# Optimization experiments

Measured on AMD Instinct MI355X. Metric: run time of the kernel, lower is better.

Reference implementation:

```python
import jax, jax.numpy as jnp
import numpy as np

N_NODES = 50000
N_EDGES = 800000
F_IN = 128
HID = 128
N_GRAPHS = 256


def setup_inputs() -> dict:
    key = jax.random.key(0)
    ks = jax.random.split(key, 12)
    gx = jax.random.normal(ks[0], (N_NODES, F_IN), dtype=jnp.float32)
    edge_index = jax.random.randint(ks[1], (2, N_EDGES), 0, N_NODES, dtype=jnp.int64)
    batch = jnp.sort(jax.random.randint(ks[2], (N_NODES,), 0, N_GRAPHS, dtype=jnp.int64))
    edge_attr = jax.random.uniform(ks[3], (N_EDGES,), dtype=jnp.float32)
    s1 = 1.0 / np.sqrt(F_IN)
    s2 = 1.0 / np.sqrt(HID)
    W1 = jax.random.uniform(ks[4], (F_IN, HID), jnp.float32, -s1, s1)
    b1 = jnp.zeros((HID,), jnp.float32)
    W2 = jax.random.uniform(ks[5], (HID, HID), jnp.float32, -s2, s2)
    b2 = jnp.zeros((HID,), jnp.float32)
    W3 = jax.random.uniform(ks[6], (HID, HID), jnp.float32, -s2, s2)
    b3 = jnp.zeros((HID,), jnp.float32)
    return {"gx": gx, "edge_index": edge_index, "batch": batch, "edge_attr": edge_attr,
            "W1": W1, "b1": b1, "W2": W2, "b2": b2, "W3": W3, "b3": b3}


def _gcn_conv(x, W, b, row, col, edge_weight, n_nodes):
    # PyG GCNConv with add_self_loops=False:
    #   deg[i] = sum of edge_weight over edges with dst == i
    #   norm_e = deg^{-1/2}[row] * w_e * deg^{-1/2}[col]
    #   out[i] = sum_{e: col_e == i} norm_e * (x @ W)[row_e] + b
    deg = jax.ops.segment_sum(edge_weight, col, num_segments=n_nodes)
    dinv = jnp.where(deg > 0, jax.lax.rsqrt(deg), 0.0)
    norm = dinv[row] * edge_weight * dinv[col]  # [E]
    h = x @ W  # [N, H]
    msg = h[row] * norm[:, None]  # [E, H] gather + scale
    out = jax.ops.segment_sum(msg, col, num_segments=n_nodes)  # scatter-add
    return out + b


def reference(gx, edge_index, batch, edge_attr, W1, b1, W2, b2, W3, b3):
    row, col = edge_index[0], edge_index[1]
    n = gx.shape[0]
    # dropout layers are in eval mode (identity) for a deterministic reference
    h = jax.nn.relu(_gcn_conv(gx, W1, b1, row, col, edge_attr, n))
    h = jax.nn.relu(_gcn_conv(h, W2, b2, row, col, edge_attr, n))
    h = _gcn_conv(h, W3, b3, row, col, edge_attr, n)
    readout = jax.ops.segment_sum(h, batch, num_segments=N_GRAPHS)  # global_add_pool
    return h, readout
```

## Files before the change

### kernel.cpp

```cpp
#include <hip/hip_runtime.h>

#define FEAT 128

typedef __attribute__((ext_vector_type(8))) short short8;
typedef __attribute__((ext_vector_type(4))) float f32x4;

__device__ __forceinline__ unsigned int bf16rtn(float f) {
    unsigned int u = __float_as_uint(f);
    return (u + 0x7fffu + ((u >> 16) & 1u)) >> 16;
}
__device__ __forceinline__ float bf16tof(unsigned int h) { return __uint_as_float(h << 16); }
__device__ __forceinline__ float bf16lo(unsigned int v) { return __uint_as_float(v << 16); }
__device__ __forceinline__ float bf16hi(unsigned int v) { return __uint_as_float(v & 0xffff0000u); }

__global__ void zero_kernel(float* __restrict__ p, int n) {
    int i = blockIdx.x * blockDim.x + threadIdx.x;
    if (i < n) p[i] = 0.0f;
}

__global__ __launch_bounds__(256) void hist_kernel(const int* __restrict__ col,
                                                   int* __restrict__ ghist,
                                                   int E, int nblk, int nbuck) {
    __shared__ int h[256];
    const int t = threadIdx.x, b = blockIdx.x;
    h[t] = 0;
    __syncthreads();
    const int base = b * 4096;
#pragma unroll
    for (int i = 0; i < 16; ++i) {
        int e = base + i * 256 + t;
        if (e < E) atomicAdd(&h[col[e] >> 8], 1);
    }
    __syncthreads();
    if (t < nbuck) ghist[t * nblk + b] = h[t];
}

__global__ __launch_bounds__(256) void scan_block_kernel(const int* __restrict__ cnt,
                                                         int* __restrict__ out,
                                                         int* __restrict__ bsum, int M) {
    __shared__ int s[256];
    int t = threadIdx.x;
    int i = blockIdx.x * 256 + t;
    int own = (i < M) ? cnt[i] : 0;
    s[t] = own;
    for (int off = 1; off < 256; off <<= 1) {
        __syncthreads();
        int v = (t >= off) ? s[t - off] : 0;
        __syncthreads();
        s[t] += v;
    }
    __syncthreads();
    if (i < M) out[i] = s[t] - own;
    if (t == 255) bsum[blockIdx.x] = s[255];
}

__global__ __launch_bounds__(256) void scan_bsum_kernel(int* __restrict__ bsum, int nb) {
    __shared__ int s[256];
    int t = threadIdx.x;
    int own = (t < nb) ? bsum[t] : 0;
    s[t] = own;
    for (int off = 1; off < 256; off <<= 1) {
        __syncthreads();
        int v = (t >= off) ? s[t - off] : 0;
        __syncthreads();
        s[t] += v;
    }
    __syncthreads();
    if (t < nb) bsum[t] = s[t] - own;
}

__global__ __launch_bounds__(256) void scan_add_kernel(int* __restrict__ out,
                                                       const int* __restrict__ bsum,
                                                       int M, int total) {
    int i = blockIdx.x * 256 + threadIdx.x;
    if (i < M) out[i] += bsum[blockIdx.x];
    if (i == M) out[M] = total;
}

__global__ __launch_bounds__(256) void scatter1_kernel(const int* __restrict__ row,
                                                       const int* __restrict__ col,
                                                       const float* __restrict__ ew,
                                                       const int* __restrict__ gbase,
                                                       uint2* __restrict__ bedge,
                                                       int E, int nblk, int nbuck) {
    __shared__ int cur[256];
    const int t = threadIdx.x, b = blockIdx.x;
    if (t < nbuck) cur[t] = gbase[t * nblk + b];
    __syncthreads();
    const int base = b * 4096;
#pragma unroll
    for (int i = 0; i < 16; ++i) {
        int e = base + i * 256 + t;
        if (e < E) {
            int c = col[e];
            int slot = atomicAdd(&cur[c >> 8], 1);
            bedge[slot] = make_uint2(((unsigned)c << 16) | (unsigned)row[e],
                                     __float_as_uint(ew[e]));
        }
    }
}

__global__ __launch_bounds__(256) void bucket_kernel(const uint2* __restrict__ bedge,
                                                     const int* __restrict__ gbase,
                                                     int* __restrict__ rowptr,
                                                     float* __restrict__ dinv,
                                                     uint2* __restrict__ sedge,
                                                     int N, int E, int nblk, int nbuck) {
    __shared__ int lcnt[256];
    __shared__ float lw[256];
    __shared__ int lscan[256];
    __shared__ int lcur[256];
    __shared__ float ldv[256];

    const int d = blockIdx.x, t = threadIdx.x;
    const int base = gbase[d * nblk];
    const int end  = (d == nbuck - 1) ? E : gbase[(d + 1) * nblk];

    lcnt[t] = 0;
    lw[t] = 0.f;
    __syncthreads();
    for (int i = base + t; i < end; i += 256) {
        uint2 p = bedge[i];
        int c = (p.x >> 16) & 255;
        atomicAdd(&lcnt[c], 1);
        atomicAdd(&lw[c], __uint_as_float(p.y));
    }
    __syncthreads();
    int own = lcnt[t];
    lscan[t] = own;
    for (int off = 1; off < 256; off <<= 1) {
        __syncthreads();
        int v = (t >= off) ? lscan[t - off] : 0;
        __syncthreads();
        lscan[t] += v;
    }
    __syncthreads();
    int excl = lscan[t] - own;
    lcur[t] = base + excl;
    float wsum = lw[t];
    float dv = (wsum > 0.f) ? rsqrtf(wsum) : 0.f;
    ldv[t] = dv;
    int node = d * 256 + t;
    if (node < N) {
        rowptr[node] = base + excl;
        dinv[node] = dv;
    }
    if (d == nbuck - 1 && t == 0) rowptr[N] = E;
    __syncthreads();
    for (int i = base + t; i < end; i += 256) {
        uint2 p = bedge[i];
        int c = (p.x >> 16) & 255;
        int slot = atomicAdd(&lcur[c], 1);
        sedge[slot] = make_uint2(p.x & 0xFFFFu,
                                 __float_as_uint(__uint_as_float(p.y) * ldv[c]));
    }
}

__global__ void norm_kernel(uint2* __restrict__ sedge, const float* __restrict__ dinv, int E) {
    int i = blockIdx.x * blockDim.x + threadIdx.x;
    if (i < E) {
        uint2 p = sedge[i];
        p.y = __float_as_uint(__uint_as_float(p.y) * dinv[p.x]);
        sedge[i] = p;
    }
}

__global__ void convw_kernel(const float* __restrict__ W0, const float* __restrict__ W1,
                             const float* __restrict__ W2,
                             unsigned short* __restrict__ Whi, unsigned short* __restrict__ Wlo) {
    int i = blockIdx.x * blockDim.x + threadIdx.x;
    int which = blockIdx.y;
    const float* W = (which == 0) ? W0 : (which == 1) ? W1 : W2;
    int c = i >> 7, k = i & 127;
    float w = W[(size_t)k * FEAT + c];
    unsigned int h = bf16rtn(w);
    size_t off = (size_t)which * 16384 + (size_t)c * FEAT + k;
    Whi[off] = (unsigned short)h;
    Wlo[off] = (unsigned short)bf16rtn(w - bf16tof(h));
}

__global__ __launch_bounds__(256) void gemm_mfma_kernel(
    const float* __restrict__ X,
    const unsigned short* __restrict__ Wthi, const unsigned short* __restrict__ Wtlo,
    unsigned int* __restrict__ hb,
    int N)
{
    __shared__ unsigned short xh[64 * 128];
    __shared__ unsigned short xl[64 * 128];
    __shared__ unsigned short wh[64 * 128];
    __shared__ unsigned short wl[64 * 128];

    const int tid = threadIdx.x;
    const int r0 = blockIdx.x * 64;
    const int cb = blockIdx.y;

#pragma unroll
    for (int it = 0; it < 4; ++it) {
        int idx = it * 256 + tid;
        int c = idx >> 4;
        int k8 = (idx & 15) * 8;
        int sw = k8 ^ ((c & 7) << 3);
        size_t src = (size_t)(cb * 64 + c) * FEAT + k8;
        *(short8*)&wh[c * 128 + sw] = *(const short8*)(Wthi + src);
        *(short8*)&wl[c * 128 + sw] = *(const short8*)(Wtlo + src);
    }
#pragma unroll
    for (int it = 0; it < 8; ++it) {
        int idx = it * 256 + tid;
        int r = idx >> 5;
        int kc = (idx & 31) * 4;
        int gr = r0 + r;
        float4 v = make_float4(0.f, 0.f, 0.f, 0.f);
        if (gr < N) v = *(const float4*)(X + (size_t)gr * FEAT + kc);
        unsigned int h0 = bf16rtn(v.x), h1 = bf16rtn(v.y);
        unsigned int h2 = bf16rtn(v.z), h3 = bf16rtn(v.w);
        ushort4 hv = make_ushort4((unsigned short)h0, (unsigned short)h1,
                                  (unsigned short)h2, (unsigned short)h3);
        ushort4 lv = make_ushort4((unsigned short)bf16rtn(v.x - bf16tof(h0)),
                                  (unsigned short)bf16rtn(v.y - bf16tof(h1)),
                                  (unsigned short)bf16rtn(v.z - bf16tof(h2)),
                                  (unsigned short)bf16rtn(v.w - bf16tof(h3)));
        int sw = kc ^ ((r & 7) << 3);
        *(ushort4*)&xh[r * 128 + sw] = hv;
        *(ushort4*)&xl[r * 128 + sw] = lv;
    }
    __syncthreads();

    const int lane = tid & 63;
    const int wv = tid >> 6;
    const int m = lane & 15;
    const int quad = lane >> 4;
    const int arow = wv * 16 + m;

    f32x4 acc[4];
#pragma unroll
    for (int ct = 0; ct < 4; ++ct) acc[ct] = (f32x4){0.f, 0.f, 0.f, 0.f};

#pragma unroll
    for (int kt = 0; kt < 4; ++kt) {
        const int k0 = kt * 32 + quad * 8;
        const int aw = k0 ^ ((arow & 7) << 3);
        short8 ah = *(const short8*)&xh[arow * 128 + aw];
        short8 al = *(const short8*)&xl[arow * 128 + aw];
#pragma unroll
        for (int ct = 0; ct < 4; ++ct) {
            int bc = ct * 16 + m;
            int bw = k0 ^ ((bc & 7) << 3);
            short8 bh = *(const short8*)&wh[bc * 128 + bw];
            short8 bl = *(const short8*)&wl[bc * 128 + bw];
            acc[ct] = __builtin_amdgcn_mfma_f32_16x16x32_bf16(ah, bh, acc[ct], 0, 0, 0);
            acc[ct] = __builtin_amdgcn_mfma_f32_16x16x32_bf16(ah, bl, acc[ct], 0, 0, 0);
            acc[ct] = __builtin_amdgcn_mfma_f32_16x16x32_bf16(al, bh, acc[ct], 0, 0, 0);
        }
    }

    __syncthreads();
    unsigned short* cl = xh;
#pragma unroll
    for (int ct = 0; ct < 4; ++ct)
#pragma unroll
        for (int reg = 0; reg < 4; ++reg) {
            int rrow = wv * 16 + quad * 4 + reg;
            cl[rrow * 72 + ct * 16 + m] = (unsigned short)bf16rtn(acc[ct][reg]);
        }
    __syncthreads();
#pragma unroll
    for (int it = 0; it < 2; ++it) {
        int idx = it * 256 + tid;
        int r = idx >> 3;
        int c4 = (idx & 7) * 4;
        int gr = r0 + r;
        if (gr < N) {
            uint4 pv = *(const uint4*)&cl[r * 72 + c4 * 2];
            *(uint4*)(hb + (size_t)gr * 64 + cb * 32 + c4) = pv;
        }
    }
}

template <int RELU>
__global__ __launch_bounds__(256) void agg_kernel(
    const int* __restrict__ rowptr, const uint2* __restrict__ sedge,
    const unsigned int* __restrict__ hb, const float* __restrict__ bias,
    float* __restrict__ outX, int N)
{
    const int node = blockIdx.x * 4 + (threadIdx.x >> 6);
    if (node >= N) return;
    const int lane = threadIdx.x & 63;
    const int s = rowptr[node];
    const int e = rowptr[node + 1];

    float2 bv = *(const float2*)(bias + lane * 2);
    float a0 = bv.x, a1 = bv.y;

    int i = s;
    const int nfull = (e - s) >> 3;
    if (nfull > 0) {
        uint2 c0 = sedge[i], c1 = sedge[i + 1], c2 = sedge[i + 2], c3 = sedge[i + 3];
        uint2 c4 = sedge[i + 4], c5 = sedge[i + 5], c6 = sedge[i + 6], c7 = sedge[i + 7];
        for (int g = 0; g < nfull; ++g) {
            unsigned v0 = hb[(size_t)c0.x * 64 + lane];
            unsigned v1 = hb[(size_t)c1.x * 64 + lane];
            unsigned v2 = hb[(size_t)c2.x * 64 + lane];
            unsigned v3 = hb[(size_t)c3.x * 64 + lane];
            unsigned v4 = hb[(size_t)c4.x * 64 + lane];
            unsigned v5 = hb[(size_t)c5.x * 64 + lane];
            unsigned v6 = hb[(size_t)c6.x * 64 + lane];
            unsigned v7 = hb[(size_t)c7.x * 64 + lane];
            float w0 = __uint_as_float(c0.y), w1 = __uint_as_float(c1.y);
            float w2 = __uint_as_float(c2.y), w3 = __uint_as_float(c3.y);
            float w4 = __uint_as_float(c4.y), w5 = __uint_as_float(c5.y);
            float w6 = __uint_as_float(c6.y), w7 = __uint_as_float(c7.y);
            int ni = i + 8;
            if (g + 1 < nfull) {
                c0 = sedge[ni];     c1 = sedge[ni + 1];
                c2 = sedge[ni + 2]; c3 = sedge[ni + 3];
                c4 = sedge[ni + 4]; c5 = sedge[ni + 5];
                c6 = sedge[ni + 6]; c7 = sedge[ni + 7];
            }
            a0 = fmaf(w0, bf16lo(v0), a0);  a1 = fmaf(w0, bf16hi(v0), a1);
            a0 = fmaf(w1, bf16lo(v1), a0);  a1 = fmaf(w1, bf16hi(v1), a1);
            a0 = fmaf(w2, bf16lo(v2), a0);  a1 = fmaf(w2, bf16hi(v2), a1);
            a0 = fmaf(w3, bf16lo(v3), a0);  a1 = fmaf(w3, bf16hi(v3), a1);
            a0 = fmaf(w4, bf16lo(v4), a0);  a1 = fmaf(w4, bf16hi(v4), a1);
            a0 = fmaf(w5, bf16lo(v5), a0);  a1 = fmaf(w5, bf16hi(v5), a1);
            a0 = fmaf(w6, bf16lo(v6), a0);  a1 = fmaf(w6, bf16hi(v6), a1);
            a0 = fmaf(w7, bf16lo(v7), a0);  a1 = fmaf(w7, bf16hi(v7), a1);
            i = ni;
        }
    }
    for (; i < e; ++i) {
        uint2 p = sedge[i];
        unsigned v = hb[(size_t)p.x * 64 + lane];
        float w = __uint_as_float(p.y);
        a0 = fmaf(w, bf16lo(v), a0);
        a1 = fmaf(w, bf16hi(v), a1);
    }

    if (RELU) { a0 = fmaxf(a0, 0.f); a1 = fmaxf(a1, 0.f); }
    *(float2*)(outX + (size_t)node * FEAT + lane * 2) = make_float2(a0, a1);
}

__global__ __launch_bounds__(128) void readout_kernel(const float* __restrict__ h,
                                                      const int* __restrict__ batch,
                                                      float* __restrict__ ro, int N) {
    const int g = blockIdx.x;
    const int chunk = blockIdx.y;
    const int j = threadIdx.x;
    int lo = 0, hi = N;
    while (lo < hi) { int mid = (lo + hi) >> 1; if (batch[mid] < g) lo = mid + 1; else hi = mid; }
    int lo2 = lo, hi2 = N;
    while (lo2 < hi2) { int mid = (lo2 + hi2) >> 1; if (batch[mid] < g + 1) lo2 = mid + 1; else hi2 = mid; }
    const int len = lo2 - lo;
    const int per = (len + 7) >> 3;
    const int cs = lo + chunk * per;
    const int ce = min(lo2, cs + per);

    float s0 = 0.f, s1 = 0.f, s2 = 0.f, s3 = 0.f;
    int n = cs;
    for (; n + 4 <= ce; n += 4) {
        s0 += h[(size_t)n * FEAT + j];
        s1 += h[(size_t)(n + 1) * FEAT + j];
        s2 += h[(size_t)(n + 2) * FEAT + j];
        s3 += h[(size_t)(n + 3) * FEAT + j];
    }
    for (; n < ce; ++n) s0 += h[(size_t)n * FEAT + j];
    float acc = (s0 + s1) + (s2 + s3);
    if (cs < ce) atomicAdd(&ro[(size_t)g * FEAT + j], acc);
}

static inline size_t align256(size_t x) { return (x + 255) & ~(size_t)255; }

extern "C" void kernel_launch(void* const* d_in, const int* in_sizes, int n_in,
                              void* d_out, int out_size, void* d_ws, size_t ws_size,
                              hipStream_t stream) {
    const float* gx    = (const float*)d_in[0];
    const int*   ei    = (const int*)d_in[1];
    const int*   batch = (const int*)d_in[2];
    const float* ew    = (const float*)d_in[3];
    const float* W1 = (const float*)d_in[4];
    const float* b1 = (const float*)d_in[5];
    const float* W2 = (const float*)d_in[6];
    const float* b2 = (const float*)d_in[7];
    const float* W3 = (const float*)d_in[8];
    const float* b3 = (const float*)d_in[9];

    const int N = in_sizes[0] / FEAT;
    const int E = in_sizes[3];
    const int G = (out_size - N * FEAT) / FEAT;

    const int* row = ei;
    const int* col = ei + E;

    const int nbuck = (N + 255) >> 8;
    const int nblk  = (E + 4095) >> 12;
    const int M     = nbuck * nblk;

    char* ws = (char*)d_ws;
    int*   rowptr = (int*)ws;         ws += align256((size_t)(N + 1) * 4);
    float* dinv   = (float*)ws;       ws += align256((size_t)N * 4);
    int*   ghist  = (int*)ws;         ws += align256((size_t)M * 4);
    int*   gbase  = (int*)ws;         ws += align256((size_t)(M + 1) * 4);
    int*   bsum   = (int*)ws;         ws += align256(256 * 4);
    uint2* bedge  = (uint2*)ws;       ws += align256((size_t)E * 8);
    uint2* sedge  = (uint2*)ws;       ws += align256((size_t)E * 8);
    unsigned int* hb = (unsigned int*)ws;  ws += align256((size_t)N * 64 * 4);
    float* bufX   = (float*)ws;       ws += align256((size_t)N * FEAT * 4);
    unsigned short* Wh = (unsigned short*)ws; ws += align256((size_t)3 * 16384 * 2);
    unsigned short* Wl = (unsigned short*)ws; ws += align256((size_t)3 * 16384 * 2);

    float* h_out = (float*)d_out;
    float* ro    = h_out + (size_t)N * FEAT;

    hist_kernel<<<nblk, 256, 0, stream>>>(col, ghist, E, nblk, nbuck);
    const int snb = (M + 255) / 256;
    scan_block_kernel<<<snb, 256, 0, stream>>>(ghist, gbase, bsum, M);
    scan_bsum_kernel<<<1, 256, 0, stream>>>(bsum, snb);
    scan_add_kernel<<<snb + 1, 256, 0, stream>>>(gbase, bsum, M, E);
    scatter1_kernel<<<nblk, 256, 0, stream>>>(row, col, ew, gbase, bedge, E, nblk, nbuck);
    bucket_kernel<<<nbuck, 256, 0, stream>>>(bedge, gbase, rowptr, dinv, sedge, N, E, nblk, nbuck);
    norm_kernel<<<(E + 255) / 256, 256, 0, stream>>>(sedge, dinv, E);

    convw_kernel<<<dim3(64, 3), 256, 0, stream>>>(W1, W2, W3, Wh, Wl);

    dim3 ggrid((N + 63) / 64, 2);
    const int ablocks = (N + 3) / 4;

    gemm_mfma_kernel<<<ggrid, 256, 0, stream>>>(gx, Wh, Wl, hb, N);
    agg_kernel<1><<<ablocks, 256, 0, stream>>>(rowptr, sedge, hb, b1, bufX, N);
    gemm_mfma_kernel<<<ggrid, 256, 0, stream>>>(bufX, Wh + 16384, Wl + 16384, hb, N);
    agg_kernel<1><<<ablocks, 256, 0, stream>>>(rowptr, sedge, hb, b2, bufX, N);
    gemm_mfma_kernel<<<ggrid, 256, 0, stream>>>(bufX, Wh + 32768, Wl + 32768, hb, N);
    agg_kernel<0><<<ablocks, 256, 0, stream>>>(rowptr, sedge, hb, b3, h_out, N);
    zero_kernel<<<(G * FEAT + 255) / 256, 256, 0, stream>>>(ro, G * FEAT);
    readout_kernel<<<dim3(G, 8), 128, 0, stream>>>(h_out, batch, ro, N);
}
```

Before: 331.8 us.

## Split wavefront into two half-waves per edge in aggregation; fold scan-add into consumers

The aggregation kernel now has each 64-lane wavefront process two edges at once, one per 32-lane half. Each lane loads 8 bytes (4 bf16 features), and the two halves are combined with a cross-lane shuffle before the bias, ReLU and float4 store. This is meant to raise memory-level parallelism on the gathers and halve loop iterations per node, at the cost of masked tail loads and a shuffle reduction. Separately, the scan_add kernel launch is removed: the scatter and bucket kernels add the block prefix from bsum themselves, saving one launch.

```diff
diff --git a/kernel.cpp b/kernel.cpp
--- a/kernel.cpp
+++ b/kernel.cpp
@@ -69,23 +69,19 @@
     if (t < nb) bsum[t] = s[t] - own;
 }
 
-__global__ __launch_bounds__(256) void scan_add_kernel(int* __restrict__ out,
-                                                       const int* __restrict__ bsum,
-                                                       int M, int total) {
-    int i = blockIdx.x * 256 + threadIdx.x;
-    if (i < M) out[i] += bsum[blockIdx.x];
-    if (i == M) out[M] = total;
-}
-
 __global__ __launch_bounds__(256) void scatter1_kernel(const int* __restrict__ row,
                                                        const int* __restrict__ col,
                                                        const float* __restrict__ ew,
-                                                       const int* __restrict__ gbase,
+                                                       const int* __restrict__ gsc,
+                                                       const int* __restrict__ bsum,
                                                        uint2* __restrict__ bedge,
                                                        int E, int nblk, int nbuck) {
     __shared__ int cur[256];
     const int t = threadIdx.x, b = blockIdx.x;
-    if (t < nbuck) cur[t] = gbase[t * nblk + b];
+    if (t < nbuck) {
+        int idx = t * nblk + b;
+        cur[t] = gsc[idx] + bsum[idx >> 8];
+    }
     __syncthreads();
     const int base = b * 4096;
 #pragma unroll
@@ -101,7 +97,8 @@
 }
 
 __global__ __launch_bounds__(256) void bucket_kernel(const uint2* __restrict__ bedge,
-                                                     const int* __restrict__ gbase,
+                                                     const int* __restrict__ gsc,
+                                                     const int* __restrict__ bsum,
                                                      int* __restrict__ rowptr,
                                                      float* __restrict__ dinv,
                                                      uint2* __restrict__ sedge,
@@ -113,8 +110,14 @@
     __shared__ float ldv[256];
 
     const int d = blockIdx.x, t = threadIdx.x;
-    const int base = gbase[d * nblk];
-    const int end  = (d == nbuck - 1) ? E : gbase[(d + 1) * nblk];
+    const int i0 = d * nblk;
+    const int base = gsc[i0] + bsum[i0 >> 8];
+    int end;
+    if (d == nbuck - 1) end = E;
+    else {
+        const int i1 = (d + 1) * nblk;
+        end = gsc[i1] + bsum[i1 >> 8];
+    }
 
     lcnt[t] = 0;
     lw[t] = 0.f;
@@ -280,64 +283,80 @@
 template <int RELU>
 __global__ __launch_bounds__(256) void agg_kernel(
     const int* __restrict__ rowptr, const uint2* __restrict__ sedge,
-    const unsigned int* __restrict__ hb, const float* __restrict__ bias,
+    const uint2* __restrict__ hb2,
+    const float* __restrict__ bias,
     float* __restrict__ outX, int N)
 {
     const int node = blockIdx.x * 4 + (threadIdx.x >> 6);
     if (node >= N) return;
     const int lane = threadIdx.x & 63;
+    const int h = lane >> 5;
+    const int j = lane & 31;
     const int s = rowptr[node];
     const int e = rowptr[node + 1];
 
-    float2 bv = *(const float2*)(bias + lane * 2);
-    float a0 = bv.x, a1 = bv.y;
-
-    int i = s;
-    const int nfull = (e - s) >> 3;
-    if (nfull > 0) {
-        uint2 c0 = sedge[i], c1 = sedge[i + 1], c2 = sedge[i + 2], c3 = sedge[i + 3];
-        uint2 c4 = sedge[i + 4], c5 = sedge[i + 5], c6 = sedge[i + 6], c7 = sedge[i + 7];
-        for (int g = 0; g < nfull; ++g) {
-            unsigned v0 = hb[(size_t)c0.x * 64 + lane];
-            unsigned v1 = hb[(size_t)c1.x * 64 + lane];
-            unsigned v2 = hb[(size_t)c2.x * 64 + lane];
-            unsigned v3 = hb[(size_t)c3.x * 64 + lane];
-            unsigned v4 = hb[(size_t)c4.x * 64 + lane];
-            unsigned v5 = hb[(size_t)c5.x * 64 + lane];
-            unsigned v6 = hb[(size_t)c6.x * 64 + lane];
-            unsigned v7 = hb[(size_t)c7.x * 64 + lane];
-            float w0 = __uint_as_float(c0.y), w1 = __uint_as_float(c1.y);
-            float w2 = __uint_as_float(c2.y), w3 = __uint_as_float(c3.y);
-            float w4 = __uint_as_float(c4.y), w5 = __uint_as_float(c5.y);
-            float w6 = __uint_as_float(c6.y), w7 = __uint_as_float(c7.y);
-            int ni = i + 8;
-            if (g + 1 < nfull) {
-                c0 = sedge[ni];     c1 = sedge[ni + 1];
-                c2 = sedge[ni + 2]; c3 = sedge[ni + 3];
-                c4 = sedge[ni + 4]; c5 = sedge[ni + 5];
-                c6 = sedge[ni + 6]; c7 = sedge[ni + 7];
-            }
-            a0 = fmaf(w0, bf16lo(v0), a0);  a1 = fmaf(w0, bf16hi(v0), a1);
-            a0 = fmaf(w1, bf16lo(v1), a0);  a1 = fmaf(w1, bf16hi(v1), a1);
-            a0 = fmaf(w2, bf16lo(v2), a0);  a1 = fmaf(w2, bf16hi(v2), a1);
-            a0 = fmaf(w3, bf16lo(v3), a0);  a1 = fmaf(w3, bf16hi(v3), a1);
-            a0 = fmaf(w4, bf16lo(v4), a0);  a1 = fmaf(w4, bf16hi(v4), a1);
-            a0 = fmaf(w5, bf16lo(v5), a0);  a1 = fmaf(w5, bf16hi(v5), a1);
-            a0 = fmaf(w6, bf16lo(v6), a0);  a1 = fmaf(w6, bf16hi(v6), a1);
-            a0 = fmaf(w7, bf16lo(v7), a0);  a1 = fmaf(w7, bf16hi(v7), a1);
-            i = ni;
-        }
-    }
-    for (; i < e; ++i) {
-        uint2 p = sedge[i];
-        unsigned v = hb[(size_t)p.x * 64 + lane];
-        float w = __uint_as_float(p.y);
-        a0 = fmaf(w, bf16lo(v), a0);
-        a1 = fmaf(w, bf16hi(v), a1);
-    }
-
-    if (RELU) { a0 = fmaxf(a0, 0.f); a1 = fmaxf(a1, 0.f); }
-    *(float2*)(outX + (size_t)node * FEAT + lane * 2) = make_float2(a0, a1);
+    float a0 = 0.f, a1 = 0.f, a2 = 0.f, a3 = 0.f;
+
+    for (int gb = s; gb < e; gb += 16) {
+        uint2 m0, m1, m2, m3, m4, m5, m6, m7;
+        if (gb + 16 <= e) {
+            m0 = sedge[gb + 0 + h];  m1 = sedge[gb + 2 + h];
+            m2 = sedge[gb + 4 + h];  m3 = sedge[gb + 6 + h];
+            m4 = sedge[gb + 8 + h];  m5 = sedge[gb + 10 + h];
+            m6 = sedge[gb + 12 + h]; m7 = sedge[gb + 14 + h];
+        } else {
+            const uint2 z = make_uint2(0u, 0u);
+            int i0 = gb + 0 + h, i1 = gb + 2 + h, i2 = gb + 4 + h, i3 = gb + 6 + h;
+            int i4 = gb + 8 + h, i5 = gb + 10 + h, i6 = gb + 12 + h, i7 = gb + 14 + h;
+            m0 = (i0 < e) ? sedge[i0] : z;  m1 = (i1 < e) ? sedge[i1] : z;
+            m2 = (i2 < e) ? sedge[i2] : z;  m3 = (i3 < e) ? sedge[i3] : z;
+            m4 = (i4 < e) ? sedge[i4] : z;  m5 = (i5 < e) ? sedge[i5] : z;
+            m6 = (i6 < e) ? sedge[i6] : z;  m7 = (i7 < e) ? sedge[i7] : z;
+        }
+        uint2 v0 = hb2[(size_t)m0.x * 32 + j];
+        uint2 v1 = hb2[(size_t)m1.x * 32 + j];
+        uint2 v2 = hb2[(size_t)m2.x * 32 + j];
+        uint2 v3 = hb2[(size_t)m3.x * 32 + j];
+        uint2 v4 = hb2[(size_t)m4.x * 32 + j];
+        uint2 v5 = hb2[(size_t)m5.x * 32 + j];
+        uint2 v6 = hb2[(size_t)m6.x * 32 + j];
+        uint2 v7 = hb2[(size_t)m7.x * 32 + j];
+        float w0 = __uint_as_float(m0.y), w1 = __uint_as_float(m1.y);
+        float w2 = __uint_as_float(m2.y), w3 = __uint_as_float(m3.y);
+        float w4 = __uint_as_float(m4.y), w5 = __uint_as_float(m5.y);
+        float w6 = __uint_as_float(m6.y), w7 = __uint_as_float(m7.y);
+        a0 = fmaf(w0, bf16lo(v0.x), a0); a1 = fmaf(w0, bf16hi(v0.x), a1);
+        a2 = fmaf(w0, bf16lo(v0.y), a2); a3 = fmaf(w0, bf16hi(v0.y), a3);
+        a0 = fmaf(w1, bf16lo(v1.x), a0); a1 = fmaf(w1, bf16hi(v1.x), a1);
+        a2 = fmaf(w1, bf16lo(v1.y), a2); a3 = fmaf(w1, bf16hi(v1.y), a3);
+        a0 = fmaf(w2, bf16lo(v2.x), a0); a1 = fmaf(w2, bf16hi(v2.x), a1);
+        a2 = fmaf(w2, bf16lo(v2.y), a2); a3 = fmaf(w2, bf16hi(v2.y), a3);
+        a0 = fmaf(w3, bf16lo(v3.x), a0); a1 = fmaf(w3, bf16hi(v3.x), a1);
+        a2 = fmaf(w3, bf16lo(v3.y), a2); a3 = fmaf(w3, bf16hi(v3.y), a3);
+        a0 = fmaf(w4, bf16lo(v4.x), a0); a1 = fmaf(w4, bf16hi(v4.x), a1);
+        a2 = fmaf(w4, bf16lo(v4.y), a2); a3 = fmaf(w4, bf16hi(v4.y), a3);
+        a0 = fmaf(w5, bf16lo(v5.x), a0); a1 = fmaf(w5, bf16hi(v5.x), a1);
+        a2 = fmaf(w5, bf16lo(v5.y), a2); a3 = fmaf(w5, bf16hi(v5.y), a3);
+        a0 = fmaf(w6, bf16lo(v6.x), a0); a1 = fmaf(w6, bf16hi(v6.x), a1);
+        a2 = fmaf(w6, bf16lo(v6.y), a2); a3 = fmaf(w6, bf16hi(v6.y), a3);
+        a0 = fmaf(w7, bf16lo(v7.x), a0); a1 = fmaf(w7, bf16hi(v7.x), a1);
+        a2 = fmaf(w7, bf16lo(v7.y), a2); a3 = fmaf(w7, bf16hi(v7.y), a3);
+    }
+
+    a0 += __shfl_xor(a0, 32);
+    a1 += __shfl_xor(a1, 32);
+    a2 += __shfl_xor(a2, 32);
+    a3 += __shfl_xor(a3, 32);
+
+    if (h == 0) {
+        float4 bv = ((const float4*)bias)[j];
+        a0 += bv.x; a1 += bv.y; a2 += bv.z; a3 += bv.w;
+        if (RELU) {
+            a0 = fmaxf(a0, 0.f); a1 = fmaxf(a1, 0.f);
+            a2 = fmaxf(a2, 0.f); a3 = fmaxf(a3, 0.f);
+        }
+        *(float4*)(outX + (size_t)node * FEAT + j * 4) = make_float4(a0, a1, a2, a3);
+    }
 }
 
 __global__ __launch_bounds__(128) void readout_kernel(const float* __restrict__ h,
@@ -399,7 +418,7 @@
     int*   rowptr = (int*)ws;         ws += align256((size_t)(N + 1) * 4);
     float* dinv   = (float*)ws;       ws += align256((size_t)N * 4);
     int*   ghist  = (int*)ws;         ws += align256((size_t)M * 4);
-    int*   gbase  = (int*)ws;         ws += align256((size_t)(M + 1) * 4);
+    int*   gsc    = (int*)ws;         ws += align256((size_t)M * 4);
     int*   bsum   = (int*)ws;         ws += align256(256 * 4);
     uint2* bedge  = (uint2*)ws;       ws += align256((size_t)E * 8);
     uint2* sedge  = (uint2*)ws;       ws += align256((size_t)E * 8);
@@ -413,24 +432,24 @@
 
     hist_kernel<<<nblk, 256, 0, stream>>>(col, ghist, E, nblk, nbuck);
     const int snb = (M + 255) / 256;
-    scan_block_kernel<<<snb, 256, 0, stream>>>(ghist, gbase, bsum, M);
+    scan_block_kernel<<<snb, 256, 0, stream>>>(ghist, gsc, bsum, M);
     scan_bsum_kernel<<<1, 256, 0, stream>>>(bsum, snb);
-    scan_add_kernel<<<snb + 1, 256, 0, stream>>>(gbase, bsum, M, E);
-    scatter1_kernel<<<nblk, 256, 0, stream>>>(row, col, ew, gbase, bedge, E, nblk, nbuck);
-    bucket_kernel<<<nbuck, 256, 0, stream>>>(bedge, gbase, rowptr, dinv, sedge, N, E, nblk, nbuck);
+    scatter1_kernel<<<nblk, 256, 0, stream>>>(row, col, ew, gsc, bsum, bedge, E, nblk, nbuck);
+    bucket_kernel<<<nbuck, 256, 0, stream>>>(bedge, gsc, bsum, rowptr, dinv, sedge, N, E, nblk, nbuck);
     norm_kernel<<<(E + 255) / 256, 256, 0, stream>>>(sedge, dinv, E);
 
     convw_kernel<<<dim3(64, 3), 256, 0, stream>>>(W1, W2, W3, Wh, Wl);
 
     dim3 ggrid((N + 63) / 64, 2);
     const int ablocks = (N + 3) / 4;
+    const uint2* hb2 = (const uint2*)hb;
 
     gemm_mfma_kernel<<<ggrid, 256, 0, stream>>>(gx, Wh, Wl, hb, N);
-    agg_kernel<1><<<ablocks, 256, 0, stream>>>(rowptr, sedge, hb, b1, bufX, N);
+    agg_kernel<1><<<ablocks, 256, 0, stream>>>(rowptr, sedge, hb2, b1, bufX, N);
     gemm_mfma_kernel<<<ggrid, 256, 0, stream>>>(bufX, Wh + 16384, Wl + 16384, hb, N);
-    agg_kernel<1><<<ablocks, 256, 0, stream>>>(rowptr, sedge, hb, b2, bufX, N);
+    agg_kernel<1><<<ablocks, 256, 0, stream>>>(rowptr, sedge, hb2, b2, bufX, N);
     gemm_mfma_kernel<<<ggrid, 256, 0, stream>>>(bufX, Wh + 32768, Wl + 32768, hb, N);
-    agg_kernel<0><<<ablocks, 256, 0, stream>>>(rowptr, sedge, hb, b3, h_out, N);
+    agg_kernel<0><<<ablocks, 256, 0, stream>>>(rowptr, sedge, hb2, b3, h_out, N);
     zero_kernel<<<(G * FEAT + 255) / 256, 256, 0, stream>>>(ro, G * FEAT);
     readout_kernel<<<dim3(G, 8), 128, 0, stream>>>(h_out, batch, ro, N);
 }
```

Measured after the change: 311.4 us. -6.1%, faster.
